# Optimization experiments

Hardware: AMD Instinct MI355X
Metric: run time of the kernel (lower is better)

## Reference

```python
import jax, jax.numpy as jnp
import numpy as np

B, S, D = 8, 2048, 512

def setup_inputs() -> dict:
    key = jax.random.key(0)
    ks = jax.random.split(key, 4)
    scale = 1.0 / np.sqrt(D)
    x = jax.random.normal(ks[0], (B, S, D), dtype=jnp.float32)
    Wq = jax.random.normal(ks[1], (D, D), dtype=jnp.float32) * scale
    Wk = jax.random.normal(ks[2], (D, D), dtype=jnp.float32) * scale
    Wv = jax.random.normal(ks[3], (D, D), dtype=jnp.float32) * scale
    bq = jnp.zeros((D,), jnp.float32)
    bk = jnp.zeros((D,), jnp.float32)
    bv = jnp.zeros((D,), jnp.float32)
    return {"x": x, "Wq": Wq, "bq": bq, "Wk": Wk, "bk": bk, "Wv": Wv, "bv": bv}

def reference(x, Wq, bq, Wk, bk, Wv, bv):
    # Q, K, V projections: [B,S,D]
    Q = jnp.einsum('bsd,de->bse', x, Wq) + bq
    K = jnp.einsum('bsd,de->bse', x, Wk) + bk
    V = jnp.einsum('bsd,de->bse', x, Wv) + bv
    scale = jnp.sqrt(jnp.asarray(Q.shape[-1], Q.dtype))
    scores = jnp.einsum('bqd,bkd->bqk', Q, K) / scale  # [B,S,S]
    attn = jax.nn.softmax(scores, axis=-1)
    context = jnp.einsum('bqk,bkd->bqd', attn, V)  # [B,S,D]
    return context
```

## Files before the change

### kernel.cpp

```cpp
#include <hip/hip_runtime.h>
#include <hip/hip_bf16.h>

#define B_ 8
#define S_ 2048
#define D_ 512

typedef __attribute__((ext_vector_type(8))) short short8;
typedef __attribute__((ext_vector_type(4))) float f32x4;

static __device__ __forceinline__ unsigned short f2bf(float f) {
    union { float f; unsigned u; } v; v.f = f;
    unsigned r = v.u + 0x7FFFu + ((v.u >> 16) & 1u);
    return (unsigned short)(r >> 16);
}

static __device__ __forceinline__ float fexp2(float x) {
    float r; asm("v_exp_f32 %0, %1" : "=v"(r) : "v"(x)); return r;
}

static __device__ __forceinline__ void gl_lds16(const void* g, void* l) {
    __builtin_amdgcn_global_load_lds(
        (const __attribute__((address_space(1))) unsigned int*)g,
        (__attribute__((address_space(3))) unsigned int*)l, 16, 0, 0);
}

__global__ void k_cvt_x(const float* __restrict__ x, unsigned short* __restrict__ xb) {
    int i = blockIdx.x * 256 + threadIdx.x;
    const float4* p = (const float4*)x + (size_t)i * 2;
    float4 a = p[0], b = p[1];
    union { unsigned short u[8]; uint4 v; } o;
    o.u[0] = f2bf(a.x); o.u[1] = f2bf(a.y); o.u[2] = f2bf(a.z); o.u[3] = f2bf(a.w);
    o.u[4] = f2bf(b.x); o.u[5] = f2bf(b.y); o.u[6] = f2bf(b.z); o.u[7] = f2bf(b.w);
    ((uint4*)xb)[i] = o.v;
}

__global__ void k_cvt_w(const float* __restrict__ Wq, const float* __restrict__ Wk,
                        const float* __restrict__ Wv, unsigned short* __restrict__ Wt) {
    int idx = blockIdx.x * 256 + threadIdx.x;
    int z = idx >> 18;
    int r = idx & 262143;
    int e = r >> 9, d = r & 511;
    const float* W = (z == 0) ? Wq : ((z == 1) ? Wk : Wv);
    Wt[idx] = f2bf(W[d * 512 + e]);
}

__global__ void k_lzero(float* __restrict__ l) {
    l[blockIdx.x * 256 + threadIdx.x] = 0.f;
}

__global__ __launch_bounds__(256, 4) void k_qkv(
    const unsigned short* __restrict__ xb, const unsigned short* __restrict__ Wt,
    const float* __restrict__ biasq, const float* __restrict__ biask,
    const float* __restrict__ biasv,
    unsigned short* __restrict__ Qb, unsigned short* __restrict__ Kb,
    unsigned short* __restrict__ Vs) {
  __shared__ __align__(16) unsigned char smA[16384];
  __shared__ __align__(16) unsigned char smB[16384];
  const int z = blockIdx.z;
  const unsigned short* W = Wt + (size_t)z * (D_ * D_);
  const int lane = threadIdx.x & 63, wid = threadIdx.x >> 6;
  const int c = lane & 15, g = lane >> 4;
  const int wr = wid >> 1, wc = wid & 1;
  const int m_blk = blockIdx.x * 128;
  const int n_blk = blockIdx.y * 128;

  const int src_sw = ((lane & 7) * 16) ^ (((lane >> 3) & 7) << 4);
  const unsigned char* ga = (const unsigned char*)xb
      + (size_t)(m_blk + wid * 32 + (lane >> 3)) * 1024;
  const unsigned char* gb = (const unsigned char*)W
      + (size_t)(n_blk + wid * 32 + (lane >> 3)) * 1024;
  unsigned char* la = smA + wid * 4096;
  unsigned char* lb = smB + wid * 4096;

  f32x4 acc[4][4];
#pragma unroll
  for (int mi = 0; mi < 4; ++mi)
#pragma unroll
    for (int ni = 0; ni < 4; ++ni) acc[mi][ni] = (f32x4){0.f, 0.f, 0.f, 0.f};

  for (int step = 0; step < 8; ++step) {
    __syncthreads();
#pragma unroll
    for (int i = 0; i < 4; ++i) {
      gl_lds16(ga + (size_t)i * 8192 + step * 128 + src_sw, la + i * 1024);
      gl_lds16(gb + (size_t)i * 8192 + step * 128 + src_sw, lb + i * 1024);
    }
    __syncthreads();
#pragma unroll
    for (int kc = 0; kc < 2; ++kc) {
      const int ro = (kc * 64 + g * 16) ^ ((c & 7) << 4);
      short8 af[4], bf[4];
#pragma unroll
      for (int mi = 0; mi < 4; ++mi)
        af[mi] = *(const short8*)(smA + (wr * 64 + mi * 16 + c) * 128 + ro);
#pragma unroll
      for (int ni = 0; ni < 4; ++ni)
        bf[ni] = *(const short8*)(smB + (wc * 64 + ni * 16 + c) * 128 + ro);
#pragma unroll
      for (int mi = 0; mi < 4; ++mi)
#pragma unroll
        for (int ni = 0; ni < 4; ++ni)
          acc[mi][ni] = __builtin_amdgcn_mfma_f32_16x16x32_bf16(af[mi], bf[ni], acc[mi][ni], 0, 0, 0);
    }
  }

  const int m0 = m_blk + wr * 64;
  const int n0 = n_blk + wc * 64;
  if (z < 2) {
    const float* bias = (z == 0) ? biasq : biask;
    unsigned short* outp = (z == 0) ? Qb : Kb;
    const float scl = (z == 0) ? 0.0637587238f : 1.0f;
#pragma unroll
    for (int ni = 0; ni < 4; ++ni) {
      int cc = n0 + ni * 16 + c;
      float bb = bias[cc];
#pragma unroll
      for (int mi = 0; mi < 4; ++mi)
#pragma unroll
        for (int r = 0; r < 4; ++r) {
          int row = m0 + mi * 16 + g * 4 + r;
          outp[(size_t)row * D_ + cc] = f2bf((acc[mi][ni][r] + bb) * scl);
        }
    }
  } else {
#pragma unroll
    for (int ni = 0; ni < 4; ++ni) {
      int e = n0 + ni * 16 + c;
      float bb = biasv[e];
#pragma unroll
      for (int mi = 0; mi < 4; ++mi) {
        int row = m0 + mi * 16 + g * 4;
        int bi = row >> 11, sl = row & 2047;
        int t = sl >> 5, kvin = sl & 31;
        union { unsigned short u[4]; uint2 v; } pk;
#pragma unroll
        for (int r = 0; r < 4; ++r) pk.u[r] = f2bf(acc[mi][ni][r] + bb);
        *(uint2*)(Vs + ((((size_t)bi * 64 + t) * 512) + e) * 32 + kvin) = pk.v;
      }
    }
  }
}

__global__ __launch_bounds__(256, 4) void k_pa(
    const unsigned short* __restrict__ Qb, const unsigned short* __restrict__ Kb,
    unsigned short* __restrict__ P, float* __restrict__ l,
    int b_base, int bc) {
  __shared__ __align__(16) unsigned char smA[16384];
  __shared__ __align__(16) unsigned char smB[16384];
  const int lane = threadIdx.x & 63, wid = threadIdx.x >> 6;
  const int c = lane & 15, g = lane >> 4;
  const int wr = wid >> 1, wc = wid & 1;
  const int bloc = blockIdx.x % bc;
  const int tile = blockIdx.x / bc;
  const int b = b_base + bloc;
  const int m_blk = (tile & 15) * 128;
  const int n_blk = (tile >> 4) * 128;
  unsigned short* Pb = P + (size_t)bloc * S_ * S_;

  const int src_sw = ((lane & 7) * 16) ^ (((lane >> 3) & 7) << 4);
  const unsigned char* ga = (const unsigned char*)(Kb + (size_t)b * S_ * D_)
      + (size_t)(m_blk + wid * 32 + (lane >> 3)) * 1024;
  const unsigned char* gb = (const unsigned char*)(Qb + (size_t)b * S_ * D_)
      + (size_t)(n_blk + wid * 32 + (lane >> 3)) * 1024;
  unsigned char* la = smA + wid * 4096;
  unsigned char* lb = smB + wid * 4096;

  f32x4 acc[4][4];
#pragma unroll
  for (int mi = 0; mi < 4; ++mi)
#pragma unroll
    for (int ni = 0; ni < 4; ++ni) acc[mi][ni] = (f32x4){0.f, 0.f, 0.f, 0.f};

  for (int step = 0; step < 8; ++step) {
    __syncthreads();
#pragma unroll
    for (int i = 0; i < 4; ++i) {
      gl_lds16(ga + (size_t)i * 8192 + step * 128 + src_sw, la + i * 1024);
      gl_lds16(gb + (size_t)i * 8192 + step * 128 + src_sw, lb + i * 1024);
    }
    __syncthreads();
#pragma unroll
    for (int kc = 0; kc < 2; ++kc) {
      const int ro = (kc * 64 + g * 16) ^ ((c & 7) << 4);
      short8 af[4], bf[4];
#pragma unroll
      for (int mi = 0; mi < 4; ++mi)
        af[mi] = *(const short8*)(smA + (wr * 64 + mi * 16 + c) * 128 + ro);
#pragma unroll
      for (int ni = 0; ni < 4; ++ni)
        bf[ni] = *(const short8*)(smB + (wc * 64 + ni * 16 + c) * 128 + ro);
#pragma unroll
      for (int mi = 0; mi < 4; ++mi)
#pragma unroll
        for (int ni = 0; ni < 4; ++ni)
          acc[mi][ni] = __builtin_amdgcn_mfma_f32_16x16x32_bf16(af[mi], bf[ni], acc[mi][ni], 0, 0, 0);
    }
  }

  const int kv0 = m_blk + wr * 64;
  const int q0  = n_blk + wc * 64;
  const float SH = 11.5415603f;
  float psum[4] = {0.f, 0.f, 0.f, 0.f};
#pragma unroll
  for (int ni = 0; ni < 4; ++ni) {
    const int q = q0 + ni * 16 + c;
#pragma unroll
    for (int mi = 0; mi < 4; ++mi) {
      float p0 = fexp2(acc[mi][ni][0] - SH);
      float p1 = fexp2(acc[mi][ni][1] - SH);
      float p2 = fexp2(acc[mi][ni][2] - SH);
      float p3 = fexp2(acc[mi][ni][3] - SH);
      psum[ni] += (p0 + p1) + (p2 + p3);
      unsigned w0, w1;
      asm("v_cvt_pk_bf16_f32 %0, %1, %2" : "=v"(w0) : "v"(p0), "v"(p1));
      asm("v_cvt_pk_bf16_f32 %0, %1, %2" : "=v"(w1) : "v"(p2), "v"(p3));
      *(uint2*)(Pb + (size_t)q * S_ + kv0 + mi * 16 + g * 4) = (uint2){w0, w1};
    }
  }
#pragma unroll
  for (int ni = 0; ni < 4; ++ni) {
    float v = psum[ni];
    v += __shfl_xor(v, 16);
    v += __shfl_xor(v, 32);
    if (g == 0)
      atomicAdd(l + b * S_ + q0 + ni * 16 + c, v);
  }
}

__global__ __launch_bounds__(256, 4) void k_pb(
    const unsigned short* __restrict__ P, const unsigned short* __restrict__ Vs,
    const float* __restrict__ l, float* __restrict__ out,
    int b_base, int bc) {
  __shared__ __align__(16) unsigned char smA[16384];
  __shared__ __align__(16) unsigned char smB[16384];
  const int lane = threadIdx.x & 63, wid = threadIdx.x >> 6;
  const int c = lane & 15, g = lane >> 4;
  const int wr = wid >> 1, wc = wid & 1;
  const int bloc = blockIdx.x % bc;
  const int tile = blockIdx.x / bc;
  const int b = b_base + bloc;
  const int m_blk = (tile & 3) * 128;
  const int n_blk = (tile >> 2) * 128;
  const unsigned short* Pb = P + (size_t)bloc * S_ * S_;
  const unsigned char* Vsb = (const unsigned char*)(Vs + (size_t)b * 64 * 512 * 32);

  const int src_sw = ((lane & 7) * 16) ^ (((lane >> 3) & 7) << 4);
  const unsigned char* ga = Vsb + (size_t)(src_sw >> 6) * 32768
      + (size_t)(m_blk + wid * 32 + (lane >> 3)) * 64 + (src_sw & 63);
  const unsigned char* gb = (const unsigned char*)Pb
      + (size_t)(n_blk + wid * 32 + (lane >> 3)) * 4096;
  unsigned char* la = smA + wid * 4096;
  unsigned char* lb = smB + wid * 4096;

  f32x4 acc[4][4];
#pragma unroll
  for (int mi = 0; mi < 4; ++mi)
#pragma unroll
    for (int ni = 0; ni < 4; ++ni) acc[mi][ni] = (f32x4){0.f, 0.f, 0.f, 0.f};

  for (int step = 0; step < 32; ++step) {
    __syncthreads();
#pragma unroll
    for (int i = 0; i < 4; ++i) {
      gl_lds16(ga + (size_t)step * 65536 + i * 512, la + i * 1024);
      gl_lds16(gb + (size_t)i * 32768 + step * 128 + src_sw, lb + i * 1024);
    }
    __syncthreads();
#pragma unroll
    for (int kc = 0; kc < 2; ++kc) {
      const int ro = (kc * 64 + g * 16) ^ ((c & 7) << 4);
      short8 af[4], bf[4];
#pragma unroll
      for (int mi = 0; mi < 4; ++mi)
        af[mi] = *(const short8*)(smA + (wr * 64 + mi * 16 + c) * 128 + ro);
#pragma unroll
      for (int ni = 0; ni < 4; ++ni)
        bf[ni] = *(const short8*)(smB + (wc * 64 + ni * 16 + c) * 128 + ro);
#pragma unroll
      for (int mi = 0; mi < 4; ++mi)
#pragma unroll
        for (int ni = 0; ni < 4; ++ni)
          acc[mi][ni] = __builtin_amdgcn_mfma_f32_16x16x32_bf16(af[mi], bf[ni], acc[mi][ni], 0, 0, 0);
    }
  }

  const int m0 = m_blk + wr * 64;
  const int n0 = n_blk + wc * 64;
  float* ob = out + (size_t)b * S_ * D_;
#pragma unroll
  for (int ni = 0; ni < 4; ++ni) {
    const int q = n0 + ni * 16 + c;
    const float inv = 1.f / l[b * S_ + q];
#pragma unroll
    for (int mi = 0; mi < 4; ++mi) {
      float4 v;
      v.x = acc[mi][ni][0] * inv; v.y = acc[mi][ni][1] * inv;
      v.z = acc[mi][ni][2] * inv; v.w = acc[mi][ni][3] * inv;
      *(float4*)(ob + (size_t)q * D_ + m0 + mi * 16 + g * 4) = v;
    }
  }
}

extern "C" void kernel_launch(void* const* d_in, const int* in_sizes, int n_in,
                              void* d_out, int out_size, void* d_ws, size_t ws_size,
                              hipStream_t stream) {
  const float* x  = (const float*)d_in[0];
  const float* Wq = (const float*)d_in[1];
  const float* bq = (const float*)d_in[2];
  const float* Wk = (const float*)d_in[3];
  const float* bk = (const float*)d_in[4];
  const float* Wv = (const float*)d_in[5];
  const float* bv = (const float*)d_in[6];
  float* out = (float*)d_out;

  unsigned short* xb = (unsigned short*)d_ws;
  unsigned short* Wt = xb + (size_t)16384 * 512;
  unsigned short* Qb = Wt + (size_t)3 * 512 * 512;
  unsigned short* Kb = Qb + (size_t)16384 * 512;
  unsigned short* Vs = Kb + (size_t)16384 * 512;
  float* l = (float*)Wt;
  unsigned short* Pfull = Vs + (size_t)8 * 64 * 512 * 32;
  const size_t full_need =
      (size_t)((unsigned char*)(Pfull + (size_t)8 * 2048 * 2048) - (unsigned char*)d_ws);

  k_cvt_x<<<dim3(4096), dim3(256), 0, stream>>>(x, xb);
  k_cvt_w<<<dim3(3072), dim3(256), 0, stream>>>(Wq, Wk, Wv, Wt);
  k_qkv<<<dim3(128, 4, 3), dim3(256), 0, stream>>>(xb, Wt, bq, bk, bv, Qb, Kb, Vs);
  k_lzero<<<dim3(64), dim3(256), 0, stream>>>(l);

  if (ws_size >= full_need) {
    k_pa<<<dim3(2048), dim3(256), 0, stream>>>(Qb, Kb, Pfull, l, 0, 8);
    k_pb<<<dim3(512),  dim3(256), 0, stream>>>(Pfull, Vs, l, out, 0, 8);
  } else {
    unsigned short* P2 = xb;
    for (int g2 = 0; g2 < 4; ++g2) {
      k_pa<<<dim3(512), dim3(256), 0, stream>>>(Qb, Kb, P2, l, g2 * 2, 2);
      k_pb<<<dim3(128), dim3(256), 0, stream>>>(P2, Vs, l, out, g2 * 2, 2);
    }
  }
}
```

Measured before the change: 133.2 us.

## Rewrite score kernel as 256x256-tile, 8-wave double-buffered pipelined GEMM

The QK^T/exp kernel now uses 512-thread blocks computing 256x256 tiles with a 128KB double-buffered LDS. Global-to-LDS loads for the next K-chunk are interleaved with MFMA phases, using explicit vmcnt waits, raw barriers and setprio. This is meant to hide load latency and raise data reuse per block. The cost is one block per CU, a large accumulator register footprint, and fewer blocks, which may hurt tail balance.

Result: slower. 138.7 us (+4.1%).

```diff
diff --git a/kernel.cpp b/kernel.cpp
--- a/kernel.cpp
+++ b/kernel.cpp
@@ -141,71 +141,113 @@
   }
 }
 
-__global__ __launch_bounds__(256, 4) void k_pa(
+__global__ __launch_bounds__(512, 1) void k_pa(
     const unsigned short* __restrict__ Qb, const unsigned short* __restrict__ Kb,
     unsigned short* __restrict__ P, float* __restrict__ l,
     int b_base, int bc) {
-  __shared__ __align__(16) unsigned char smA[16384];
-  __shared__ __align__(16) unsigned char smB[16384];
+  __shared__ __align__(16) unsigned char sm[131072];
   const int lane = threadIdx.x & 63, wid = threadIdx.x >> 6;
   const int c = lane & 15, g = lane >> 4;
-  const int wr = wid >> 1, wc = wid & 1;
+  const int wm = wid >> 2, wn = wid & 3;
   const int bloc = blockIdx.x % bc;
   const int tile = blockIdx.x / bc;
   const int b = b_base + bloc;
-  const int m_blk = (tile & 15) * 128;
-  const int n_blk = (tile >> 4) * 128;
+  const int m_blk = (tile & 7) * 256;
+  const int n_blk = (tile >> 3) * 256;
   unsigned short* Pb = P + (size_t)bloc * S_ * S_;
 
-  const int src_sw = ((lane & 7) * 16) ^ (((lane >> 3) & 7) << 4);
-  const unsigned char* ga = (const unsigned char*)(Kb + (size_t)b * S_ * D_)
-      + (size_t)(m_blk + wid * 32 + (lane >> 3)) * 1024;
-  const unsigned char* gb = (const unsigned char*)(Qb + (size_t)b * S_ * D_)
-      + (size_t)(n_blk + wid * 32 + (lane >> 3)) * 1024;
-  unsigned char* la = smA + wid * 4096;
-  unsigned char* lb = smB + wid * 4096;
-
-  f32x4 acc[4][4];
-#pragma unroll
-  for (int mi = 0; mi < 4; ++mi)
+  const unsigned char* gA = (const unsigned char*)(Kb + (size_t)b * S_ * D_)
+      + (size_t)m_blk * 1024;
+  const unsigned char* gB = (const unsigned char*)(Qb + (size_t)b * S_ * D_)
+      + (size_t)n_blk * 1024;
+  const int swsrc = ((lane & 7) * 16) ^ (((lane >> 3) & 7) << 4);
+  const int ksw = (c & 7) << 4;
+
+  f32x4 acc[8][4];
+#pragma unroll
+  for (int mi = 0; mi < 8; ++mi)
 #pragma unroll
     for (int ni = 0; ni < 4; ++ni) acc[mi][ni] = (f32x4){0.f, 0.f, 0.f, 0.f};
 
-  for (int step = 0; step < 8; ++step) {
-    __syncthreads();
-#pragma unroll
-    for (int i = 0; i < 4; ++i) {
-      gl_lds16(ga + (size_t)i * 8192 + step * 128 + src_sw, la + i * 1024);
-      gl_lds16(gb + (size_t)i * 8192 + step * 128 + src_sw, lb + i * 1024);
-    }
-    __syncthreads();
-#pragma unroll
-    for (int kc = 0; kc < 2; ++kc) {
-      const int ro = (kc * 64 + g * 16) ^ ((c & 7) << 4);
-      short8 af[4], bf[4];
-#pragma unroll
-      for (int mi = 0; mi < 4; ++mi)
-        af[mi] = *(const short8*)(smA + (wr * 64 + mi * 16 + c) * 128 + ro);
-#pragma unroll
-      for (int ni = 0; ni < 4; ++ni)
-        bf[ni] = *(const short8*)(smB + (wc * 64 + ni * 16 + c) * 128 + ro);
-#pragma unroll
-      for (int mi = 0; mi < 4; ++mi)
-#pragma unroll
-        for (int ni = 0; ni < 4; ++ni)
-          acc[mi][ni] = __builtin_amdgcn_mfma_f32_16x16x32_bf16(af[mi], bf[ni], acc[mi][ni], 0, 0, 0);
-    }
-  }
-
-  const int kv0 = m_blk + wr * 64;
-  const int q0  = n_blk + wc * 64;
+#define STG(mat_, half_, t_)                                                 \
+  if ((t_) < 8) {                                                            \
+    const unsigned char* gsrc = (mat_) ? gB : gA;                            \
+    const int r0_ = (mat_) ? ((half_) * 32 + (wid >> 1) * 64 + (wid & 1) * 16) \
+                           : ((half_) * 64 + (wid >> 2) * 128 + (wid & 3) * 16); \
+    unsigned char* ldst = sm + (((t_) & 1) ? 65536 : 0)                      \
+                          + ((mat_) ? 32768 : 0) + r0_ * 128;                \
+    gl_lds16(gsrc + (size_t)(r0_ + (lane >> 3)) * 1024 + (t_) * 128 + swsrc, ldst); \
+    gl_lds16(gsrc + (size_t)(r0_ + 8 + (lane >> 3)) * 1024 + (t_) * 128 + swsrc, ldst + 1024); \
+  }
+
+#define PHASE(T_, mih_, nih_, STAGE_, WAIT_)                                 \
+  {                                                                          \
+    const unsigned char* Ab = sm + (((T_) & 1) ? 65536 : 0);                 \
+    const unsigned char* Bb = Ab + 32768;                                    \
+    short8 af[4][2], bf[2][2];                                               \
+    _Pragma("unroll")                                                        \
+    for (int mi = 0; mi < 4; ++mi) {                                         \
+      int row = wm * 128 + (mih_) * 64 + mi * 16 + c;                        \
+      af[mi][0] = *(const short8*)(Ab + row * 128 + ((g * 16) ^ ksw));       \
+      af[mi][1] = *(const short8*)(Ab + row * 128 + ((64 + g * 16) ^ ksw));  \
+    }                                                                        \
+    _Pragma("unroll")                                                        \
+    for (int ni = 0; ni < 2; ++ni) {                                         \
+      int row = wn * 64 + (nih_) * 32 + ni * 16 + c;                         \
+      bf[ni][0] = *(const short8*)(Bb + row * 128 + ((g * 16) ^ ksw));       \
+      bf[ni][1] = *(const short8*)(Bb + row * 128 + ((64 + g * 16) ^ ksw));  \
+    }                                                                        \
+    STAGE_;                                                                  \
+    __builtin_amdgcn_s_barrier();                                            \
+    __builtin_amdgcn_s_setprio(1);                                           \
+    _Pragma("unroll")                                                        \
+    for (int kc = 0; kc < 2; ++kc)                                           \
+      _Pragma("unroll")                                                      \
+      for (int mi = 0; mi < 4; ++mi)                                         \
+        _Pragma("unroll")                                                    \
+        for (int ni = 0; ni < 2; ++ni)                                       \
+          acc[(mih_) * 4 + mi][(nih_) * 2 + ni] =                            \
+              __builtin_amdgcn_mfma_f32_16x16x32_bf16(                       \
+                  af[mi][kc], bf[ni][kc],                                    \
+                  acc[(mih_) * 4 + mi][(nih_) * 2 + ni], 0, 0, 0);           \
+    __builtin_amdgcn_s_setprio(0);                                           \
+    WAIT_;                                                                   \
+    __builtin_amdgcn_s_barrier();                                            \
+  }
+
+  STG(0, 0, 0); STG(1, 0, 0); STG(0, 1, 0); STG(1, 1, 0);
+  STG(0, 0, 1); STG(1, 0, 1);
+  asm volatile("s_waitcnt vmcnt(4)" ::: "memory");
+  __builtin_amdgcn_s_barrier();
+
+  for (int i = 0; i < 4; ++i) {
+    const int T0 = 2 * i, T1 = 2 * i + 1;
+    PHASE(T0, 0, 0, STG(0, 1, T1), );
+    PHASE(T0, 0, 1, STG(1, 1, T1), );
+    PHASE(T0, 1, 0, STG(0, 0, T0 + 2), );
+    if (i < 3) {
+      PHASE(T0, 1, 1, STG(1, 0, T0 + 2),
+            asm volatile("s_waitcnt vmcnt(4)" ::: "memory"));
+    } else {
+      PHASE(T0, 1, 1, ,
+            asm volatile("s_waitcnt vmcnt(0)" ::: "memory"));
+    }
+    PHASE(T1, 0, 0, STG(0, 1, T0 + 2), );
+    PHASE(T1, 0, 1, STG(1, 1, T0 + 2), );
+    PHASE(T1, 1, 0, STG(0, 0, T0 + 3), );
+    PHASE(T1, 1, 1, STG(1, 0, T0 + 3),
+          asm volatile("s_waitcnt vmcnt(4)" ::: "memory"));
+  }
+
+  const int kv0 = m_blk + wm * 128;
+  const int q0 = n_blk + wn * 64;
   const float SH = 11.5415603f;
   float psum[4] = {0.f, 0.f, 0.f, 0.f};
 #pragma unroll
   for (int ni = 0; ni < 4; ++ni) {
     const int q = q0 + ni * 16 + c;
 #pragma unroll
-    for (int mi = 0; mi < 4; ++mi) {
+    for (int mi = 0; mi < 8; ++mi) {
       float p0 = fexp2(acc[mi][ni][0] - SH);
       float p1 = fexp2(acc[mi][ni][1] - SH);
       float p2 = fexp2(acc[mi][ni][2] - SH);
@@ -225,6 +267,8 @@
     if (g == 0)
       atomicAdd(l + b * S_ + q0 + ni * 16 + c, v);
   }
+#undef STG
+#undef PHASE
 }
 
 __global__ __launch_bounds__(256, 4) void k_pb(
@@ -329,12 +373,12 @@
   k_lzero<<<dim3(64), dim3(256), 0, stream>>>(l);
 
   if (ws_size >= full_need) {
-    k_pa<<<dim3(2048), dim3(256), 0, stream>>>(Qb, Kb, Pfull, l, 0, 8);
-    k_pb<<<dim3(512),  dim3(256), 0, stream>>>(Pfull, Vs, l, out, 0, 8);
+    k_pa<<<dim3(512), dim3(512), 0, stream>>>(Qb, Kb, Pfull, l, 0, 8);
+    k_pb<<<dim3(512), dim3(256), 0, stream>>>(Pfull, Vs, l, out, 0, 8);
   } else {
     unsigned short* P2 = xb;
     for (int g2 = 0; g2 < 4; ++g2) {
-      k_pa<<<dim3(512), dim3(256), 0, stream>>>(Qb, Kb, P2, l, g2 * 2, 2);
+      k_pa<<<dim3(128), dim3(512), 0, stream>>>(Qb, Kb, P2, l, g2 * 2, 2);
       k_pb<<<dim3(128), dim3(256), 0, stream>>>(P2, Vs, l, out, g2 * 2, 2);
     }
   }
```

## Double-buffer LDS tiles in all three GEMM kernels to overlap loads with MFMA

Applied to the files above, without the earlier changes.

Doubles the shared-memory tile buffers in the QKV projection, score/exp, and PV kernels and prefetches the next K-step into the alternate buffer while the current one feeds the MFMAs. This removes one barrier per step and aims to hide global-to-LDS load latency. LDS use per block doubles to 64KB, which may cut occupancy below the launch-bounds target of 4 blocks per CU. Correctness relies on the single trailing barrier also covering completion of the async global_load_lds before the buffer is read.

Measured after the change: 161.4 us. 21.1% more time.

```diff
diff --git a/kernel.cpp b/kernel.cpp
--- a/kernel.cpp
+++ b/kernel.cpp
@@ -54,8 +54,8 @@
     const float* __restrict__ biasv,
     unsigned short* __restrict__ Qb, unsigned short* __restrict__ Kb,
     unsigned short* __restrict__ Vs) {
-  __shared__ __align__(16) unsigned char smA[16384];
-  __shared__ __align__(16) unsigned char smB[16384];
+  __shared__ __align__(16) unsigned char smA[2][16384];
+  __shared__ __align__(16) unsigned char smB[2][16384];
   const int z = blockIdx.z;
   const unsigned short* W = Wt + (size_t)z * (D_ * D_);
   const int lane = threadIdx.x & 63, wid = threadIdx.x >> 6;
@@ -69,8 +69,17 @@
       + (size_t)(m_blk + wid * 32 + (lane >> 3)) * 1024;
   const unsigned char* gb = (const unsigned char*)W
       + (size_t)(n_blk + wid * 32 + (lane >> 3)) * 1024;
-  unsigned char* la = smA + wid * 4096;
-  unsigned char* lb = smB + wid * 4096;
+
+#define STAGE1(st_, bp_)                                                     \
+  {                                                                          \
+    _Pragma("unroll")                                                        \
+    for (int i = 0; i < 4; ++i) {                                            \
+      gl_lds16(ga + (size_t)i * 8192 + (st_) * 128 + src_sw,                 \
+               smA[bp_] + wid * 4096 + i * 1024);                            \
+      gl_lds16(gb + (size_t)i * 8192 + (st_) * 128 + src_sw,                 \
+               smB[bp_] + wid * 4096 + i * 1024);                            \
+    }                                                                        \
+  }
 
   f32x4 acc[4][4];
 #pragma unroll
@@ -78,31 +87,30 @@
 #pragma unroll
     for (int ni = 0; ni < 4; ++ni) acc[mi][ni] = (f32x4){0.f, 0.f, 0.f, 0.f};
 
+  STAGE1(0, 0);
+  __syncthreads();
   for (int step = 0; step < 8; ++step) {
-    __syncthreads();
-#pragma unroll
-    for (int i = 0; i < 4; ++i) {
-      gl_lds16(ga + (size_t)i * 8192 + step * 128 + src_sw, la + i * 1024);
-      gl_lds16(gb + (size_t)i * 8192 + step * 128 + src_sw, lb + i * 1024);
-    }
-    __syncthreads();
+    const int cb = step & 1;
+    if (step < 7) STAGE1(step + 1, cb ^ 1);
 #pragma unroll
     for (int kc = 0; kc < 2; ++kc) {
       const int ro = (kc * 64 + g * 16) ^ ((c & 7) << 4);
       short8 af[4], bf[4];
 #pragma unroll
       for (int mi = 0; mi < 4; ++mi)
-        af[mi] = *(const short8*)(smA + (wr * 64 + mi * 16 + c) * 128 + ro);
+        af[mi] = *(const short8*)(smA[cb] + (wr * 64 + mi * 16 + c) * 128 + ro);
 #pragma unroll
       for (int ni = 0; ni < 4; ++ni)
-        bf[ni] = *(const short8*)(smB + (wc * 64 + ni * 16 + c) * 128 + ro);
+        bf[ni] = *(const short8*)(smB[cb] + (wc * 64 + ni * 16 + c) * 128 + ro);
 #pragma unroll
       for (int mi = 0; mi < 4; ++mi)
 #pragma unroll
         for (int ni = 0; ni < 4; ++ni)
           acc[mi][ni] = __builtin_amdgcn_mfma_f32_16x16x32_bf16(af[mi], bf[ni], acc[mi][ni], 0, 0, 0);
     }
-  }
+    __syncthreads();
+  }
+#undef STAGE1
 
   const int m0 = m_blk + wr * 64;
   const int n0 = n_blk + wc * 64;
@@ -145,8 +153,8 @@
     const unsigned short* __restrict__ Qb, const unsigned short* __restrict__ Kb,
     unsigned short* __restrict__ P, float* __restrict__ l,
     int b_base, int bc) {
-  __shared__ __align__(16) unsigned char smA[16384];
-  __shared__ __align__(16) unsigned char smB[16384];
+  __shared__ __align__(16) unsigned char smA[2][16384];
+  __shared__ __align__(16) unsigned char smB[2][16384];
   const int lane = threadIdx.x & 63, wid = threadIdx.x >> 6;
   const int c = lane & 15, g = lane >> 4;
   const int wr = wid >> 1, wc = wid & 1;
@@ -162,8 +170,17 @@
       + (size_t)(m_blk + wid * 32 + (lane >> 3)) * 1024;
   const unsigned char* gb = (const unsigned char*)(Qb + (size_t)b * S_ * D_)
       + (size_t)(n_blk + wid * 32 + (lane >> 3)) * 1024;
-  unsigned char* la = smA + wid * 4096;
-  unsigned char* lb = smB + wid * 4096;
+
+#define STAGE2(st_, bp_)                                                     \
+  {                                                                          \
+    _Pragma("unroll")                                                        \
+    for (int i = 0; i < 4; ++i) {                                            \
+      gl_lds16(ga + (size_t)i * 8192 + (st_) * 128 + src_sw,                 \
+               smA[bp_] + wid * 4096 + i * 1024);                            \
+      gl_lds16(gb + (size_t)i * 8192 + (st_) * 128 + src_sw,                 \
+               smB[bp_] + wid * 4096 + i * 1024);                            \
+    }                                                                        \
+  }
 
   f32x4 acc[4][4];
 #pragma unroll
@@ -171,31 +188,30 @@
 #pragma unroll
     for (int ni = 0; ni < 4; ++ni) acc[mi][ni] = (f32x4){0.f, 0.f, 0.f, 0.f};
 
+  STAGE2(0, 0);
+  __syncthreads();
   for (int step = 0; step < 8; ++step) {
-    __syncthreads();
-#pragma unroll
-    for (int i = 0; i < 4; ++i) {
-      gl_lds16(ga + (size_t)i * 8192 + step * 128 + src_sw, la + i * 1024);
-      gl_lds16(gb + (size_t)i * 8192 + step * 128 + src_sw, lb + i * 1024);
-    }
-    __syncthreads();
+    const int cb = step & 1;
+    if (step < 7) STAGE2(step + 1, cb ^ 1);
 #pragma unroll
     for (int kc = 0; kc < 2; ++kc) {
       const int ro = (kc * 64 + g * 16) ^ ((c & 7) << 4);
       short8 af[4], bf[4];
 #pragma unroll
       for (int mi = 0; mi < 4; ++mi)
-        af[mi] = *(const short8*)(smA + (wr * 64 + mi * 16 + c) * 128 + ro);
+        af[mi] = *(const short8*)(smA[cb] + (wr * 64 + mi * 16 + c) * 128 + ro);
 #pragma unroll
       for (int ni = 0; ni < 4; ++ni)
-        bf[ni] = *(const short8*)(smB + (wc * 64 + ni * 16 + c) * 128 + ro);
+        bf[ni] = *(const short8*)(smB[cb] + (wc * 64 + ni * 16 + c) * 128 + ro);
 #pragma unroll
       for (int mi = 0; mi < 4; ++mi)
 #pragma unroll
         for (int ni = 0; ni < 4; ++ni)
           acc[mi][ni] = __builtin_amdgcn_mfma_f32_16x16x32_bf16(af[mi], bf[ni], acc[mi][ni], 0, 0, 0);
     }
-  }
+    __syncthreads();
+  }
+#undef STAGE2
 
   const int kv0 = m_blk + wr * 64;
   const int q0  = n_blk + wc * 64;
@@ -231,8 +247,8 @@
     const unsigned short* __restrict__ P, const unsigned short* __restrict__ Vs,
     const float* __restrict__ l, float* __restrict__ out,
     int b_base, int bc) {
-  __shared__ __align__(16) unsigned char smA[16384];
-  __shared__ __align__(16) unsigned char smB[16384];
+  __shared__ __align__(16) unsigned char smA[2][16384];
+  __shared__ __align__(16) unsigned char smB[2][16384];
   const int lane = threadIdx.x & 63, wid = threadIdx.x >> 6;
   const int c = lane & 15, g = lane >> 4;
   const int wr = wid >> 1, wc = wid & 1;
@@ -249,8 +265,17 @@
       + (size_t)(m_blk + wid * 32 + (lane >> 3)) * 64 + (src_sw & 63);
   const unsigned char* gb = (const unsigned char*)Pb
       + (size_t)(n_blk + wid * 32 + (lane >> 3)) * 4096;
-  unsigned char* la = smA + wid * 4096;
-  unsigned char* lb = smB + wid * 4096;
+
+#define STAGE3(st_, bp_)                                                     \
+  {                                                                          \
+    _Pragma("unroll")                                                        \
+    for (int i = 0; i < 4; ++i) {                                            \
+      gl_lds16(ga + (size_t)(st_) * 65536 + i * 512,                         \
+               smA[bp_] + wid * 4096 + i * 1024);                            \
+      gl_lds16(gb + (size_t)i * 32768 + (st_) * 128 + src_sw,                \
+               smB[bp_] + wid * 4096 + i * 1024);                            \
+    }                                                                        \
+  }
 
   f32x4 acc[4][4];
 #pragma unroll
@@ -258,31 +283,30 @@
 #pragma unroll
     for (int ni = 0; ni < 4; ++ni) acc[mi][ni] = (f32x4){0.f, 0.f, 0.f, 0.f};
 
+  STAGE3(0, 0);
+  __syncthreads();
   for (int step = 0; step < 32; ++step) {
-    __syncthreads();
-#pragma unroll
-    for (int i = 0; i < 4; ++i) {
-      gl_lds16(ga + (size_t)step * 65536 + i * 512, la + i * 1024);
-      gl_lds16(gb + (size_t)i * 32768 + step * 128 + src_sw, lb + i * 1024);
-    }
-    __syncthreads();
+    const int cb = step & 1;
+    if (step < 31) STAGE3(step + 1, cb ^ 1);
 #pragma unroll
     for (int kc = 0; kc < 2; ++kc) {
       const int ro = (kc * 64 + g * 16) ^ ((c & 7) << 4);
       short8 af[4], bf[4];
 #pragma unroll
       for (int mi = 0; mi < 4; ++mi)
-        af[mi] = *(const short8*)(smA + (wr * 64 + mi * 16 + c) * 128 + ro);
+        af[mi] = *(const short8*)(smA[cb] + (wr * 64 + mi * 16 + c) * 128 + ro);
 #pragma unroll
       for (int ni = 0; ni < 4; ++ni)
-        bf[ni] = *(const short8*)(smB + (wc * 64 + ni * 16 + c) * 128 + ro);
+        bf[ni] = *(const short8*)(smB[cb] + (wc * 64 + ni * 16 + c) * 128 + ro);
 #pragma unroll
       for (int mi = 0; mi < 4; ++mi)
 #pragma unroll
         for (int ni = 0; ni < 4; ++ni)
           acc[mi][ni] = __builtin_amdgcn_mfma_f32_16x16x32_bf16(af[mi], bf[ni], acc[mi][ni], 0, 0, 0);
     }
-  }
+    __syncthreads();
+  }
+#undef STAGE3
 
   const int m0 = m_blk + wr * 64;
   const int n0 = n_blk + wc * 64;
```

## Merge prep kernels and enlarge P·V tile to 256x128 with 512 threads

Applied to the files above, without the earlier changes.

The x conversion, weight transpose/convert and row-sum zeroing kernels are merged into one launch, and the row-sum buffer gets its own workspace slot instead of aliasing the weight buffer. The P·V kernel now uses 8 waves per block with a 256x128 output tile covering half of D. This halves how many times each block of the large P matrix is re-read from memory and removes two kernel launches. In exchange each block needs more LDS, there are fewer blocks and occupancy is lower.

Measured after the change: 139.5 us. 1.05x slower.

```diff
diff --git a/kernel.cpp b/kernel.cpp
--- a/kernel.cpp
+++ b/kernel.cpp
@@ -24,28 +24,30 @@
         (__attribute__((address_space(3))) unsigned int*)l, 16, 0, 0);
 }
 
-__global__ void k_cvt_x(const float* __restrict__ x, unsigned short* __restrict__ xb) {
-    int i = blockIdx.x * 256 + threadIdx.x;
-    const float4* p = (const float4*)x + (size_t)i * 2;
-    float4 a = p[0], b = p[1];
-    union { unsigned short u[8]; uint4 v; } o;
-    o.u[0] = f2bf(a.x); o.u[1] = f2bf(a.y); o.u[2] = f2bf(a.z); o.u[3] = f2bf(a.w);
-    o.u[4] = f2bf(b.x); o.u[5] = f2bf(b.y); o.u[6] = f2bf(b.z); o.u[7] = f2bf(b.w);
-    ((uint4*)xb)[i] = o.v;
-}
-
-__global__ void k_cvt_w(const float* __restrict__ Wq, const float* __restrict__ Wk,
-                        const float* __restrict__ Wv, unsigned short* __restrict__ Wt) {
-    int idx = blockIdx.x * 256 + threadIdx.x;
-    int z = idx >> 18;
-    int r = idx & 262143;
-    int e = r >> 9, d = r & 511;
-    const float* W = (z == 0) ? Wq : ((z == 1) ? Wk : Wv);
-    Wt[idx] = f2bf(W[d * 512 + e]);
-}
-
-__global__ void k_lzero(float* __restrict__ l) {
-    l[blockIdx.x * 256 + threadIdx.x] = 0.f;
+__global__ void k_prep(const float* __restrict__ x,
+                       const float* __restrict__ Wq, const float* __restrict__ Wk,
+                       const float* __restrict__ Wv,
+                       unsigned short* __restrict__ xb, unsigned short* __restrict__ Wt,
+                       float* __restrict__ l) {
+    int bid = blockIdx.x;
+    if (bid < 4096) {
+        int i = bid * 256 + threadIdx.x;
+        const float4* p = (const float4*)x + (size_t)i * 2;
+        float4 a = p[0], b = p[1];
+        union { unsigned short u[8]; uint4 v; } o;
+        o.u[0] = f2bf(a.x); o.u[1] = f2bf(a.y); o.u[2] = f2bf(a.z); o.u[3] = f2bf(a.w);
+        o.u[4] = f2bf(b.x); o.u[5] = f2bf(b.y); o.u[6] = f2bf(b.z); o.u[7] = f2bf(b.w);
+        ((uint4*)xb)[i] = o.v;
+    } else if (bid < 7168) {
+        int idx = (bid - 4096) * 256 + threadIdx.x;
+        int z = idx >> 18;
+        int r = idx & 262143;
+        int e = r >> 9, d = r & 511;
+        const float* W = (z == 0) ? Wq : ((z == 1) ? Wk : Wv);
+        Wt[idx] = f2bf(W[d * 512 + e]);
+    } else {
+        l[(bid - 7168) * 256 + threadIdx.x] = 0.f;
+    }
 }
 
 __global__ __launch_bounds__(256, 4) void k_qkv(
@@ -227,11 +229,11 @@
   }
 }
 
-__global__ __launch_bounds__(256, 4) void k_pb(
+__global__ __launch_bounds__(512, 2) void k_pb(
     const unsigned short* __restrict__ P, const unsigned short* __restrict__ Vs,
     const float* __restrict__ l, float* __restrict__ out,
     int b_base, int bc) {
-  __shared__ __align__(16) unsigned char smA[16384];
+  __shared__ __align__(16) unsigned char smA[32768];
   __shared__ __align__(16) unsigned char smB[16384];
   const int lane = threadIdx.x & 63, wid = threadIdx.x >> 6;
   const int c = lane & 15, g = lane >> 4;
@@ -239,8 +241,8 @@
   const int bloc = blockIdx.x % bc;
   const int tile = blockIdx.x / bc;
   const int b = b_base + bloc;
-  const int m_blk = (tile & 3) * 128;
-  const int n_blk = (tile >> 2) * 128;
+  const int m_blk = (tile & 1) * 256;
+  const int n_blk = (tile >> 1) * 128;
   const unsigned short* Pb = P + (size_t)bloc * S_ * S_;
   const unsigned char* Vsb = (const unsigned char*)(Vs + (size_t)b * 64 * 512 * 32);
 
@@ -248,9 +250,9 @@
   const unsigned char* ga = Vsb + (size_t)(src_sw >> 6) * 32768
       + (size_t)(m_blk + wid * 32 + (lane >> 3)) * 64 + (src_sw & 63);
   const unsigned char* gb = (const unsigned char*)Pb
-      + (size_t)(n_blk + wid * 32 + (lane >> 3)) * 4096;
+      + (size_t)(n_blk + wid * 16 + (lane >> 3)) * 4096;
   unsigned char* la = smA + wid * 4096;
-  unsigned char* lb = smB + wid * 4096;
+  unsigned char* lb = smB + wid * 2048;
 
   f32x4 acc[4][4];
 #pragma unroll
@@ -261,10 +263,11 @@
   for (int step = 0; step < 32; ++step) {
     __syncthreads();
 #pragma unroll
-    for (int i = 0; i < 4; ++i) {
+    for (int i = 0; i < 4; ++i)
       gl_lds16(ga + (size_t)step * 65536 + i * 512, la + i * 1024);
+#pragma unroll
+    for (int i = 0; i < 2; ++i)
       gl_lds16(gb + (size_t)i * 32768 + step * 128 + src_sw, lb + i * 1024);
-    }
     __syncthreads();
 #pragma unroll
     for (int kc = 0; kc < 2; ++kc) {
@@ -318,24 +321,25 @@
   unsigned short* Qb = Wt + (size_t)3 * 512 * 512;
   unsigned short* Kb = Qb + (size_t)16384 * 512;
   unsigned short* Vs = Kb + (size_t)16384 * 512;
-  float* l = (float*)Wt;
-  unsigned short* Pfull = Vs + (size_t)8 * 64 * 512 * 32;
+  float* l = (float*)(Vs + (size_t)8 * 64 * 512 * 32);
+  unsigned short* Pfull = (unsigned short*)(l + 8 * 2048);
   const size_t full_need =
       (size_t)((unsigned char*)(Pfull + (size_t)8 * 2048 * 2048) - (unsigned char*)d_ws);
-
-  k_cvt_x<<<dim3(4096), dim3(256), 0, stream>>>(x, xb);
-  k_cvt_w<<<dim3(3072), dim3(256), 0, stream>>>(Wq, Wk, Wv, Wt);
+  const size_t part_need =
+      (size_t)((unsigned char*)(l + 8 * 2048) - (unsigned char*)d_ws);
+  (void)part_need;
+
+  k_prep<<<dim3(7232), dim3(256), 0, stream>>>(x, Wq, Wk, Wv, xb, Wt, l);
   k_qkv<<<dim3(128, 4, 3), dim3(256), 0, stream>>>(xb, Wt, bq, bk, bv, Qb, Kb, Vs);
-  k_lzero<<<dim3(64), dim3(256), 0, stream>>>(l);
 
   if (ws_size >= full_need) {
     k_pa<<<dim3(2048), dim3(256), 0, stream>>>(Qb, Kb, Pfull, l, 0, 8);
-    k_pb<<<dim3(512),  dim3(256), 0, stream>>>(Pfull, Vs, l, out, 0, 8);
+    k_pb<<<dim3(256),  dim3(512), 0, stream>>>(Pfull, Vs, l, out, 0, 8);
   } else {
     unsigned short* P2 = xb;
     for (int g2 = 0; g2 < 4; ++g2) {
       k_pa<<<dim3(512), dim3(256), 0, stream>>>(Qb, Kb, P2, l, g2 * 2, 2);
-      k_pb<<<dim3(128), dim3(256), 0, stream>>>(P2, Vs, l, out, g2 * 2, 2);
-    }
-  }
-}
+      k_pb<<<dim3(64), dim3(512), 0, stream>>>(P2, Vs, l, out, g2 * 2, 2);
+    }
+  }
+}
```
